# Kernel optimization log

Measured on AMD Instinct MI355X. Metric: run time of the kernel, lower is better.

Reference implementation:

```python
import jax, jax.numpy as jnp
import numpy as np

NUM_HEADS = 12


def setup_inputs() -> dict:
    key = jax.random.key(0)
    ks = jax.random.split(key, 5)
    B, N, C = 2, 256, 768
    x = jax.random.normal(ks[0], (B, N, C), dtype=jnp.float32)
    d = jax.random.normal(ks[1], (B, N, N, C), dtype=jnp.float32)
    w_qkv = jax.random.normal(ks[2], (3 * C, C), dtype=jnp.float32) * 0.02
    w_proj = jax.random.normal(ks[3], (C, C), dtype=jnp.float32) * 0.02
    b_proj = jnp.zeros((C,), dtype=jnp.float32)
    return {"x": x, "d": d, "w_qkv": w_qkv, "w_proj": w_proj, "b_proj": b_proj}


def reference(x, d, w_qkv, w_proj, b_proj):
    B, N, C = x.shape
    H = NUM_HEADS
    hd = C // H
    scale = hd ** -0.5
    # qkv projection (no bias, matching qkv_bias=False)
    qkv = x @ w_qkv.T                                   # [B, N, 3C]
    qkv = qkv.reshape(B, N, 3, H, hd).transpose(2, 0, 3, 1, 4)  # [3, B, H, N, hd]
    q, k, v = qkv[0] * scale, qkv[1], qkv[2]
    attn = jax.nn.softmax(jnp.einsum('bhid,bhjd->bhij', q, k), axis=-1)
    # pairwise bias per head: d -> [B, H, N, N, hd]
    dh = d.reshape(B, N, N, H, hd).transpose(0, 3, 1, 2, 4)
    # sum_j attn[...,j] * (v[j] + d[i,j]) split into the two terms
    out = jnp.einsum('bhij,bhjd->bhid', attn, v) \
        + jnp.einsum('bhij,bhijd->bhid', attn, dh)       # [B, H, N, hd]
    out = out.transpose(0, 2, 1, 3).reshape(B, N, C)
    return out @ w_proj.T + b_proj
```

## Files before the change

### kernel.cpp

```cpp
#include <hip/hip_runtime.h>

typedef __bf16 bf16_t;
typedef bf16_t bf16x8 __attribute__((ext_vector_type(8)));
typedef bf16_t bf16x4 __attribute__((ext_vector_type(4)));
typedef float f32x4 __attribute__((ext_vector_type(4)));

__device__ inline bf16x8 ld8(const float* p) {
    f32x4 a = *reinterpret_cast<const f32x4*>(p);
    f32x4 b = *reinterpret_cast<const f32x4*>(p + 4);
    bf16x8 r = { (bf16_t)a[0], (bf16_t)a[1], (bf16_t)a[2], (bf16_t)a[3],
                 (bf16_t)b[0], (bf16_t)b[1], (bf16_t)b[2], (bf16_t)b[3] };
    return r;
}
__device__ inline bf16x8 ld8(const bf16_t* p) {
    return *reinterpret_cast<const bf16x8*>(p);
}

template <typename AT, typename BT, typename OUT_T, bool HAS_BIAS>
__global__ __launch_bounds__(256) void gemm_bt(
    const AT* __restrict__ A, const BT* __restrict__ B,
    OUT_T* __restrict__ C, const float* __restrict__ bias,
    int K, int lda, int ldb, int ldc)
{
    const int l  = blockIdx.x;
    const int lp = (l & 7) * (gridDim.x >> 3) + (l >> 3);
    const int m0 = (lp & 7) * 64;
    const int n0 = (lp >> 3) * 64;

    __shared__ __align__(16) bf16_t As[64][72];
    __shared__ __align__(16) bf16_t Bs[64][72];

    const int tid  = threadIdx.x;
    const int lane = tid & 63;
    const int wave = tid >> 6;
    const int srow = tid >> 3;
    const int soff = (tid & 7) * 8;

    bf16x8 rA0, rA1, rB0, rB1;
    rA0 = ld8(&A[(long)(m0 + srow)      * lda + soff]);
    rA1 = ld8(&A[(long)(m0 + srow + 32) * lda + soff]);
    rB0 = ld8(&B[(long)(n0 + srow)      * ldb + soff]);
    rB1 = ld8(&B[(long)(n0 + srow + 32) * ldb + soff]);

    f32x4 acc[4] = {};

    for (int k0 = 0; k0 < K; k0 += 64) {
        *reinterpret_cast<bf16x8*>(&As[srow][soff])      = rA0;
        *reinterpret_cast<bf16x8*>(&As[srow + 32][soff]) = rA1;
        *reinterpret_cast<bf16x8*>(&Bs[srow][soff])      = rB0;
        *reinterpret_cast<bf16x8*>(&Bs[srow + 32][soff]) = rB1;
        __syncthreads();

        if (k0 + 64 < K) {
            rA0 = ld8(&A[(long)(m0 + srow)      * lda + k0 + 64 + soff]);
            rA1 = ld8(&A[(long)(m0 + srow + 32) * lda + k0 + 64 + soff]);
            rB0 = ld8(&B[(long)(n0 + srow)      * ldb + k0 + 64 + soff]);
            rB1 = ld8(&B[(long)(n0 + srow + 32) * ldb + k0 + 64 + soff]);
        }

#pragma unroll
        for (int ks = 0; ks < 64; ks += 32) {
            bf16x8 af = *reinterpret_cast<const bf16x8*>(&As[wave * 16 + (lane & 15)][(lane >> 4) * 8 + ks]);
#pragma unroll
            for (int nf = 0; nf < 4; ++nf) {
                bf16x8 bfr = *reinterpret_cast<const bf16x8*>(&Bs[nf * 16 + (lane & 15)][(lane >> 4) * 8 + ks]);
                acc[nf] = __builtin_amdgcn_mfma_f32_16x16x32_bf16(af, bfr, acc[nf], 0, 0, 0);
            }
        }
        __syncthreads();
    }

    const int crow0 = m0 + wave * 16 + (lane >> 4) * 4;
    const int ccol0 = n0 + (lane & 15);
#pragma unroll
    for (int nf = 0; nf < 4; ++nf) {
        const int col = ccol0 + nf * 16;
        const float bv = HAS_BIAS ? bias[col] : 0.0f;
#pragma unroll
        for (int v = 0; v < 4; ++v) {
            C[(long)(crow0 + v) * ldc + col] = (OUT_T)(acc[nf][v] + bv);
        }
    }
}

__global__ __launch_bounds__(256) void qk_softmax(
    const bf16_t* __restrict__ qkv,
    bf16_t* __restrict__ probs)
{
    const int bh = blockIdx.x;
    const int b = bh / 12, h = bh % 12;
    const int m0 = blockIdx.y * 64;
    const bf16_t* qbase = qkv + (long)b * 589824 + h * 64;
    const bf16_t* kbase = qkv + (long)b * 589824 + 768 + h * 64;

    __shared__ __align__(16) bf16_t Qs[64][72];
    __shared__ __align__(16) bf16_t Ks[256][72];

    const int t = threadIdx.x;
#pragma unroll
    for (int c = 0; c < 2; ++c) {
        const int chunk = c * 256 + t;
        const int row = chunk >> 3, off = (chunk & 7) * 8;
        *reinterpret_cast<uint4*>(&Qs[row][off]) =
            *reinterpret_cast<const uint4*>(qbase + (long)(m0 + row) * 2304 + off);
    }
#pragma unroll
    for (int c = 0; c < 8; ++c) {
        const int chunk = c * 256 + t;
        const int row = chunk >> 3, off = (chunk & 7) * 8;
        *reinterpret_cast<uint4*>(&Ks[row][off]) =
            *reinterpret_cast<const uint4*>(kbase + (long)row * 2304 + off);
    }
    __syncthreads();

    const int lane = t & 63, wave = t >> 6;
    f32x4 acc[16] = {};
#pragma unroll
    for (int ks = 0; ks < 64; ks += 32) {
        bf16x8 af = *reinterpret_cast<const bf16x8*>(&Qs[wave * 16 + (lane & 15)][(lane >> 4) * 8 + ks]);
#pragma unroll
        for (int nf = 0; nf < 16; ++nf) {
            bf16x8 bfr = *reinterpret_cast<const bf16x8*>(&Ks[nf * 16 + (lane & 15)][(lane >> 4) * 8 + ks]);
            acc[nf] = __builtin_amdgcn_mfma_f32_16x16x32_bf16(af, bfr, acc[nf], 0, 0, 0);
        }
    }

    float inv[4];
#pragma unroll
    for (int v = 0; v < 4; ++v) {
        float mm = -1e30f;
#pragma unroll
        for (int nf = 0; nf < 16; ++nf) { acc[nf][v] *= 0.125f; mm = fmaxf(mm, acc[nf][v]); }
#pragma unroll
        for (int o = 1; o < 16; o <<= 1) mm = fmaxf(mm, __shfl_xor(mm, o));
        float s = 0.0f;
#pragma unroll
        for (int nf = 0; nf < 16; ++nf) { float e = __expf(acc[nf][v] - mm); acc[nf][v] = e; s += e; }
#pragma unroll
        for (int o = 1; o < 16; o <<= 1) s += __shfl_xor(s, o);
        inv[v] = 1.0f / s;
    }

    bf16_t* prow = probs + ((long)bh * 256 + m0 + wave * 16 + (lane >> 4) * 4) * 256 + (lane & 15);
#pragma unroll
    for (int nf = 0; nf < 16; ++nf) {
#pragma unroll
        for (int v = 0; v < 4; ++v) {
            prow[(long)v * 256 + nf * 16] = (bf16_t)(acc[nf][v] * inv[v]);
        }
    }
}

__global__ __launch_bounds__(256) void attnd_kernel(
    const bf16_t* __restrict__ attn,
    const bf16_t* __restrict__ qkv,
    const float* __restrict__ d,
    bf16_t* __restrict__ oh)
{
    const int bi = blockIdx.x;
    const int b  = bi >> 8;
    const int i  = bi & 255;
    const int cc = blockIdx.y;
    const int t  = threadIdx.x;
    const int lane = t & 63, wave = t >> 6;

    __shared__ float attn_s[4 * 257];
    __shared__ f32x4 partial[3][64];

#pragma unroll
    for (int q = 0; q < 4; ++q) {
        attn_s[q * 257 + t] = (float)attn[(((long)(b * 12 + cc * 4 + q)) * 256 + i) * 256 + t];
    }
    __syncthreads();

    const int c0 = cc * 256 + lane * 4;
    const float* arow = attn_s + (lane >> 4) * 257;
    const int jb = wave * 64;
    const f32x4* dp = reinterpret_cast<const f32x4*>(d + (long)bi * 196608 + (long)jb * 768 + c0);
    const bf16_t* vp = qkv + (long)b * 589824 + (long)jb * 2304 + 1536 + c0;

    f32x4 acc = {};
#pragma unroll 8
    for (int jj = 0; jj < 64; ++jj) {
        f32x4 dv = __builtin_nontemporal_load(dp + (long)jj * 192);
        bf16x4 vv = *reinterpret_cast<const bf16x4*>(vp + (long)jj * 2304);
        float a = arow[jb + jj];
        acc[0] = fmaf(a, dv[0] + (float)vv[0], acc[0]);
        acc[1] = fmaf(a, dv[1] + (float)vv[1], acc[1]);
        acc[2] = fmaf(a, dv[2] + (float)vv[2], acc[2]);
        acc[3] = fmaf(a, dv[3] + (float)vv[3], acc[3]);
    }

    if (wave) partial[wave - 1][lane] = acc;
    __syncthreads();
    if (wave == 0) {
        acc += partial[0][lane] + partial[1][lane] + partial[2][lane];
        bf16x4 o = { (bf16_t)acc[0], (bf16_t)acc[1], (bf16_t)acc[2], (bf16_t)acc[3] };
        *reinterpret_cast<bf16x4*>(oh + (long)bi * 768 + c0) = o;
    }
}

extern "C" void kernel_launch(void* const* d_in, const int* in_sizes, int n_in,
                              void* d_out, int out_size, void* d_ws, size_t ws_size,
                              hipStream_t stream) {
    const float* x      = (const float*)d_in[0];
    const float* d      = (const float*)d_in[1];
    const float* w_qkv  = (const float*)d_in[2];
    const float* w_proj = (const float*)d_in[3];
    const float* b_proj = (const float*)d_in[4];
    float* out = (float*)d_out;

    char* ws = (char*)d_ws;
    bf16_t* qkvb  = (bf16_t*)(ws);
    bf16_t* probs = (bf16_t*)(ws + 2359296);
    bf16_t* oh    = (bf16_t*)(ws + 5505024);

    gemm_bt<float, float, bf16_t, false><<<288, 256, 0, stream>>>(
        x, w_qkv, qkvb, nullptr, 768, 768, 768, 2304);

    qk_softmax<<<dim3(24, 4), 256, 0, stream>>>(qkvb, probs);

    attnd_kernel<<<dim3(512, 3), 256, 0, stream>>>(probs, qkvb, d, oh);

    gemm_bt<bf16_t, float, float, true><<<96, 256, 0, stream>>>(
        oh, w_proj, out, b_proj, 768, 768, 768, 768);
}
```

Before: 99.30 us.

## Fuse output projection into attention-bias kernel via atomic accumulation

The separate output-projection GEMM is removed. Each attnd block now multiplies its 256-channel slice of the attention output by the matching slice of a bf16 copy of w_proj and atomically adds the partial results into the output. The QKV GEMM also converts w_proj to bf16 and initialises the output with the bias. This saves a kernel launch and the round trip of the intermediate tensor, at the cost of scalar (non-MFMA) dot products per block, repeated reads of w_proj by every block, and float atomics whose summation order is non-deterministic.

```diff
diff --git a/kernel.cpp b/kernel.cpp
--- a/kernel.cpp
+++ b/kernel.cpp
@@ -16,12 +16,21 @@
     return *reinterpret_cast<const bf16x8*>(p);
 }
 
-template <typename AT, typename BT, typename OUT_T, bool HAS_BIAS>
+template <typename AT, typename BT, typename OUT_T, bool SIDE>
 __global__ __launch_bounds__(256) void gemm_bt(
     const AT* __restrict__ A, const BT* __restrict__ B,
-    OUT_T* __restrict__ C, const float* __restrict__ bias,
-    int K, int lda, int ldb, int ldc)
+    OUT_T* __restrict__ C,
+    int K, int lda, int ldb, int ldc,
+    const float* __restrict__ wp_src, bf16_t* __restrict__ wp_dst,
+    float* __restrict__ out_init, const float* __restrict__ bias_init)
 {
+    if (SIDE) {
+        const int g = blockIdx.x * 256 + threadIdx.x;
+        *reinterpret_cast<bf16x8*>(wp_dst + g * 8) = ld8(wp_src + g * 8);
+        for (int e = g; e < 393216; e += 73728)
+            out_init[e] = bias_init[e % 768];
+    }
+
     const int l  = blockIdx.x;
     const int lp = (l & 7) * (gridDim.x >> 3) + (l >> 3);
     const int m0 = (lp & 7) * 64;
@@ -75,10 +84,9 @@
 #pragma unroll
     for (int nf = 0; nf < 4; ++nf) {
         const int col = ccol0 + nf * 16;
-        const float bv = HAS_BIAS ? bias[col] : 0.0f;
 #pragma unroll
         for (int v = 0; v < 4; ++v) {
-            C[(long)(crow0 + v) * ldc + col] = (OUT_T)(acc[nf][v] + bv);
+            C[(long)(crow0 + v) * ldc + col] = (OUT_T)(acc[nf][v]);
         }
     }
 }
@@ -155,7 +163,8 @@
     const bf16_t* __restrict__ attn,
     const bf16_t* __restrict__ qkv,
     const float* __restrict__ d,
-    bf16_t* __restrict__ oh)
+    const bf16_t* __restrict__ wpb,
+    float* __restrict__ out)
 {
     const int bi = blockIdx.x;
     const int b  = bi >> 8;
@@ -165,7 +174,8 @@
     const int lane = t & 63, wave = t >> 6;
 
     __shared__ float attn_s[4 * 257];
-    __shared__ f32x4 partial[3][64];
+    __shared__ float pw[4][256];
+    __shared__ float oh_lds[256];
 
 #pragma unroll
     for (int q = 0; q < 4; ++q) {
@@ -191,12 +201,26 @@
         acc[3] = fmaf(a, dv[3] + (float)vv[3], acc[3]);
     }
 
-    if (wave) partial[wave - 1][lane] = acc;
-    __syncthreads();
-    if (wave == 0) {
-        acc += partial[0][lane] + partial[1][lane] + partial[2][lane];
-        bf16x4 o = { (bf16_t)acc[0], (bf16_t)acc[1], (bf16_t)acc[2], (bf16_t)acc[3] };
-        *reinterpret_cast<bf16x4*>(oh + (long)bi * 768 + c0) = o;
+#pragma unroll
+    for (int e = 0; e < 4; ++e) pw[wave][lane * 4 + e] = acc[e];
+    __syncthreads();
+
+    oh_lds[t] = pw[0][t] + pw[1][t] + pw[2][t] + pw[3][t];
+    __syncthreads();
+
+#pragma unroll
+    for (int r = 0; r < 3; ++r) {
+        const int n = r * 256 + t;
+        const bf16_t* wp = wpb + (long)n * 768 + cc * 256;
+        float s = 0.0f;
+#pragma unroll
+        for (int c8 = 0; c8 < 32; ++c8) {
+            bf16x8 w = *reinterpret_cast<const bf16x8*>(wp + c8 * 8);
+#pragma unroll
+            for (int u = 0; u < 8; ++u)
+                s = fmaf(oh_lds[c8 * 8 + u], (float)w[u], s);
+        }
+        atomicAdd(out + (long)bi * 768 + n, s);
     }
 }
 
@@ -213,15 +237,12 @@
     char* ws = (char*)d_ws;
     bf16_t* qkvb  = (bf16_t*)(ws);
     bf16_t* probs = (bf16_t*)(ws + 2359296);
-    bf16_t* oh    = (bf16_t*)(ws + 5505024);
-
-    gemm_bt<float, float, bf16_t, false><<<288, 256, 0, stream>>>(
-        x, w_qkv, qkvb, nullptr, 768, 768, 768, 2304);
+    bf16_t* wpb   = (bf16_t*)(ws + 5505024);
+
+    gemm_bt<float, float, bf16_t, true><<<288, 256, 0, stream>>>(
+        x, w_qkv, qkvb, 768, 768, 768, 2304, w_proj, wpb, out, b_proj);
 
     qk_softmax<<<dim3(24, 4), 256, 0, stream>>>(qkvb, probs);
 
-    attnd_kernel<<<dim3(512, 3), 256, 0, stream>>>(probs, qkvb, d, oh);
-
-    gemm_bt<bf16_t, float, float, true><<<96, 256, 0, stream>>>(
-        oh, w_proj, out, b_proj, 768, 768, 768, 768);
-}
+    attnd_kernel<<<dim3(512, 3), 256, 0, stream>>>(probs, qkvb, d, wpb, out);
+}
```

Result: slower. 230.0 us (+131.6%).
